# Optimization experiments

Measured on AMD Instinct MI355X. Metric: run time of the kernel, lower is better.

The kernel has to match this reference:

```python
import jax, jax.numpy as jnp
import numpy as np

N = 100_000      # nodes
E = 1_600_000    # directed edges (before self-loops)
F_IN = 128       # input node features
H = 4            # attention heads
C = 64           # hidden channels (concat=False -> heads averaged)
NEG_SLOPE = 0.2
BN_EPS = 1e-5


def setup_inputs() -> dict:
    key = jax.random.key(0)
    ks = jax.random.split(key, 16)
    s = 0.05
    return {
        "x": jax.random.normal(ks[0], (N, F_IN), dtype=jnp.float32),
        "edge_index": jax.random.randint(ks[1], (2, E), 0, N, dtype=jnp.int64),
        # GAT layer params: layer 0 has F_IN inputs, layers 1..2 have C inputs
        "W0": jax.random.normal(ks[2], (F_IN, H * C), dtype=jnp.float32) * s,
        "Wl": jax.random.normal(ks[3], (2, C, H * C), dtype=jnp.float32) * s,
        "att_src": jax.random.normal(ks[4], (3, H, C), dtype=jnp.float32) * s,
        "att_dst": jax.random.normal(ks[5], (3, H, C), dtype=jnp.float32) * s,
        "conv_bias": jnp.zeros((3, C), dtype=jnp.float32),
        # BatchNorm1d (inference: running stats)
        "bn_gamma": jnp.ones((3, C), dtype=jnp.float32),
        "bn_beta": jnp.zeros((3, C), dtype=jnp.float32),
        "bn_mean": jax.random.normal(ks[6], (3, C), dtype=jnp.float32) * 0.1,
        "bn_var": jax.random.uniform(ks[7], (3, C), dtype=jnp.float32, minval=0.5, maxval=1.5),
        # MLP head
        "lin1_w": jax.random.normal(ks[8], (C, C // 2), dtype=jnp.float32) * s,
        "lin1_b": jnp.zeros((C // 2,), dtype=jnp.float32),
        "lin2_w": jax.random.normal(ks[9], (C // 2, 1), dtype=jnp.float32) * s,
        "lin2_b": jnp.zeros((1,), dtype=jnp.float32),
    }


def _gat_layer(x, src, dst, W, a_src, a_dst, bias):
    # x: [N, Fin] -> h: [N, H, C]
    h = (x @ W).reshape(-1, H, C)
    # per-node attention logits, gathered per edge: [Etot, H]
    e_src = jnp.einsum("nhc,hc->nh", h, a_src)
    e_dst = jnp.einsum("nhc,hc->nh", h, a_dst)
    e = jax.nn.leaky_relu(e_src[src] + e_dst[dst], NEG_SLOPE)
    # softmax over incoming edges of each target node (self-loops guarantee non-empty)
    e_max = jax.ops.segment_max(e, dst, num_segments=N)
    w = jnp.exp(e - e_max[dst])                              # [Etot, H]
    denom = jax.ops.segment_sum(w, dst, num_segments=N)      # [N, H]
    # weighted scatter-add of gathered source features
    msg = h[src] * w[:, :, None]                             # [Etot, H, C]
    out = jax.ops.segment_sum(msg, dst, num_segments=N)      # [N, H, C]
    out = out / denom[:, :, None]
    return out.mean(axis=1) + bias                           # concat=False -> head mean


def reference(x, edge_index, W0, Wl, att_src, att_dst, conv_bias,
              bn_gamma, bn_beta, bn_mean, bn_var,
              lin1_w, lin1_b, lin2_w, lin2_b):
    # add self-loops (PyG GATConv default)
    loop = jnp.arange(N, dtype=edge_index.dtype)
    src = jnp.concatenate([edge_index[0], loop])
    dst = jnp.concatenate([edge_index[1], loop])

    Ws = [W0, Wl[0], Wl[1]]
    for l in range(3):
        x = _gat_layer(x, src, dst, Ws[l], att_src[l], att_dst[l], conv_bias[l])
        x = (x - bn_mean[l]) * (bn_gamma[l] / jnp.sqrt(bn_var[l] + BN_EPS)) + bn_beta[l]
        x = jax.nn.relu(x)  # dropout is identity in inference

    x = jax.nn.relu(x @ lin1_w + lin1_b)
    x = x @ lin2_w + lin2_b
    return x.squeeze(-1)
```

## Files before the change

### kernel.cpp

```cpp
#include <hip/hip_runtime.h>
#include <hip/hip_bf16.h>
#include <cstdint>

#define N_NODES 100000
#define N_EDGES 1600000
#define N_TOT   1700000
#define HEADS   4
#define CH      64
#define HC      256
#define NEG     0.2f
#define BNEPS   1e-5f
#define NPART   8
#define PART_N  12500
#define CHUNK_E 16384

typedef __attribute__((ext_vector_type(8))) short short8;
typedef __attribute__((ext_vector_type(4))) float f32x4;

static __device__ __forceinline__ float lrelu(float x) {
    return x > 0.f ? x : NEG * x;
}
static __device__ __forceinline__ unsigned short f2bf(float f) {
    unsigned int u = __float_as_uint(f);
    unsigned int r = (u + 0x7fffu + ((u >> 16) & 1u)) >> 16;
    return (unsigned short)r;
}
static __device__ __forceinline__ float bflo(unsigned int v) { return __uint_as_float(v << 16); }
static __device__ __forceinline__ float bfhi(unsigned int v) { return __uint_as_float(v & 0xffff0000u); }

__global__ void detect_dtype(const int* ei32, int* flag) {
    int l = threadIdx.x;
    int v = ei32[2 * l + 1];
    unsigned long long b = __ballot(v == 0);
    if (l == 0) *flag = (__popcll(b) >= 48) ? 1 : 0;
}

static __device__ __forceinline__ int edge_at(const void* ei, int is64, long long pos) {
    if (is64) return (int)((const long long*)ei)[pos];
    return ((const int*)ei)[pos];
}

__global__ void convert_hist_k(const void* ei, const int* flag,
                               int* __restrict__ src32, int* __restrict__ dst32,
                               int* __restrict__ counts) {
    int e = blockIdx.x * 256 + threadIdx.x;
    if (e >= N_TOT) return;
    int is64 = *flag;
    int s, d;
    if (e < N_EDGES) { s = edge_at(ei, is64, e); d = edge_at(ei, is64, (long long)N_EDGES + e); }
    else { int v = e - N_EDGES; s = v; d = v; }
    src32[e] = s; dst32[e] = d;
    atomicAdd(&counts[d], 1);
}

__global__ void scan_block(const int* in, int* out, int* bsum) {
    __shared__ int sm[256];
    int t = threadIdx.x;
    int i = blockIdx.x * 256 + t;
    int v = (i < N_NODES) ? in[i] : 0;
    int acc = v;
    sm[t] = v; __syncthreads();
    for (int d = 1; d < 256; d <<= 1) {
        int add = (t >= d) ? sm[t - d] : 0;
        __syncthreads();
        acc += add; sm[t] = acc;
        __syncthreads();
    }
    if (i < N_NODES) out[i] = acc - v;
    if (t == 255) bsum[blockIdx.x] = acc;
}

__global__ void scan_bsum(int* bsum, int nb) {
    __shared__ int sm[512];
    int t = threadIdx.x;
    int v = (t < nb) ? bsum[t] : 0;
    int acc = v;
    sm[t] = v; __syncthreads();
    for (int d = 1; d < 512; d <<= 1) {
        int add = (t >= d) ? sm[t - d] : 0;
        __syncthreads();
        acc += add; sm[t] = acc;
        __syncthreads();
    }
    if (t < nb) bsum[t] = acc - v;
}

__global__ void scan_add(int* off, const int* bsum, int* fill) {
    int i = blockIdx.x * 256 + threadIdx.x;
    if (i < N_NODES) {
        int v = off[i] + bsum[blockIdx.x];
        off[i] = v; fill[i] = v;
    }
    if (i == 0) off[N_NODES] = N_TOT;
}

__global__ void scatter_part_k(const int* __restrict__ src32, const int* __restrict__ dst32,
                               int* __restrict__ fill, int* __restrict__ csr) {
    int part = blockIdx.x & (NPART - 1), chunk = blockIdx.x / NPART;
    int lo = part * PART_N, hi = lo + PART_N;
    int base = chunk * CHUNK_E;
    int end = min(base + CHUNK_E, N_TOT);
    for (int i = base + threadIdx.x; i < end; i += 256) {
        int d = dst32[i];
        if (d >= lo && d < hi) {
            int s = src32[i];
            int pos = atomicAdd(&fill[d], 1);
            csr[pos] = s;
        }
    }
}

template<int K>
__global__ __launch_bounds__(256) void gemm_mfma_k(const float* __restrict__ A,
                                                   const float* __restrict__ Wf,
                                                   const float* __restrict__ as,
                                                   const float* __restrict__ ad,
                                                   unsigned short* __restrict__ hb,
                                                   float* __restrict__ es,
                                                   float* __restrict__ ed) {
    __shared__ unsigned short Bs[256 * K];
    __shared__ unsigned short As[64 * K];
    int t = threadIdx.x;
    int bm = blockIdx.x * 64;

    for (int idx4 = t; idx4 < K * 64; idx4 += 256) {
        int k = idx4 >> 6;
        int c = (idx4 & 63) * 4;
        float4 wv = *(const float4*)(Wf + (size_t)k * HC + c);
        Bs[((c + 0) * K + k) ^ ((((c + 0) & 7)) << 3)] = f2bf(wv.x);
        Bs[((c + 1) * K + k) ^ ((((c + 1) & 7)) << 3)] = f2bf(wv.y);
        Bs[((c + 2) * K + k) ^ ((((c + 2) & 7)) << 3)] = f2bf(wv.z);
        Bs[((c + 3) * K + k) ^ ((((c + 3) & 7)) << 3)] = f2bf(wv.w);
    }
    {
        int row = t >> 2, seg = t & 3;
        int grow = bm + row;
        const float* Ar = A + (size_t)grow * K + seg * (K / 4);
        #pragma unroll
        for (int f = 0; f < K / 16; ++f) {
            float4 v = make_float4(0.f, 0.f, 0.f, 0.f);
            if (grow < N_NODES) v = *(const float4*)(Ar + f * 4);
            ushort4 b;
            b.x = f2bf(v.x); b.y = f2bf(v.y); b.z = f2bf(v.z); b.w = f2bf(v.w);
            int idx = (row * K + seg * (K / 4) + f * 4) ^ ((row & 7) << 3);
            *(ushort4*)(&As[idx]) = b;
        }
    }
    __syncthreads();

    int w = t >> 6, lane = t & 63;
    int c16 = lane & 15, kg = lane >> 4;
    int swz = (c16 & 7) << 3;
    f32x4 acc[4][4];
    #pragma unroll
    for (int i = 0; i < 4; ++i)
        #pragma unroll
        for (int j = 0; j < 4; ++j) acc[i][j] = (f32x4)(0.f);

    #pragma unroll
    for (int kc = 0; kc < K / 32; ++kc) {
        int ko = kc * 32 + kg * 8;
        short8 af[4], bf[4];
        #pragma unroll
        for (int rs = 0; rs < 4; ++rs)
            af[rs] = *(const short8*)(&As[((16 * rs + c16) * K + ko) ^ swz]);
        #pragma unroll
        for (int ct = 0; ct < 4; ++ct) {
            int col = w * 64 + ct * 16 + c16;
            bf[ct] = *(const short8*)(&Bs[(col * K + ko) ^ swz]);
        }
        #pragma unroll
        for (int rs = 0; rs < 4; ++rs)
            #pragma unroll
            for (int ct = 0; ct < 4; ++ct)
                acc[rs][ct] = __builtin_amdgcn_mfma_f32_16x16x32_bf16(af[rs], bf[ct], acc[rs][ct], 0, 0, 0);
    }

    float asv[4], adv[4];
    #pragma unroll
    for (int ct = 0; ct < 4; ++ct) {
        asv[ct] = as[w * 64 + ct * 16 + c16];
        adv[ct] = ad[w * 64 + ct * 16 + c16];
    }
    #pragma unroll
    for (int rs = 0; rs < 4; ++rs) {
        float esr[4], edr[4];
        #pragma unroll
        for (int reg = 0; reg < 4; ++reg) {
            float s = 0.f, d = 0.f;
            #pragma unroll
            for (int ct = 0; ct < 4; ++ct) {
                s += acc[rs][ct][reg] * asv[ct];
                d += acc[rs][ct][reg] * adv[ct];
            }
            #pragma unroll
            for (int sh = 1; sh < 16; sh <<= 1) {
                s += __shfl_xor(s, sh);
                d += __shfl_xor(d, sh);
            }
            esr[reg] = s; edr[reg] = d;
        }
        int r0 = bm + rs * 16 + kg * 4;
        if (c16 == 0) {
            #pragma unroll
            for (int reg = 0; reg < 4; ++reg) {
                if (r0 + reg < N_NODES) {
                    es[(size_t)(r0 + reg) * 4 + w] = esr[reg];
                    ed[(size_t)(r0 + reg) * 4 + w] = edr[reg];
                }
            }
        }
        #pragma unroll
        for (int ct = 0; ct < 4; ++ct)
            #pragma unroll
            for (int reg = 0; reg < 4; ++reg) {
                int grow = r0 + reg;
                if (grow < N_NODES)
                    hb[(size_t)grow * HC + w * 64 + ct * 16 + c16] = f2bf(acc[rs][ct][reg]);
            }
    }
}

__global__ __launch_bounds__(256) void aggregate_k(const unsigned short* __restrict__ h,
                                                   const float* __restrict__ es,
                                                   const float* __restrict__ ed,
                                                   const int* __restrict__ off,
                                                   const int* __restrict__ csr,
                                                   const float* __restrict__ bias,
                                                   const float* __restrict__ g,
                                                   const float* __restrict__ bb,
                                                   const float* __restrict__ mu,
                                                   const float* __restrict__ var,
                                                   float* __restrict__ xout) {
    __shared__ float wbuf[4][64][4];
    __shared__ int   sbuf[4][64];
    int wv = threadIdx.x >> 6;
    int lane = threadIdx.x & 63;
    int wid = blockIdx.x * 4 + wv;
    if (wid >= N_NODES) return;

    int s0 = off[wid], s1 = off[wid + 1];
    float4 edv = *(const float4*)(ed + (size_t)wid * 4);

    int half = lane >> 5;
    int sub  = lane & 31;
    int head = sub >> 3;
    float ds0 = 0.f, ds1 = 0.f, ds2 = 0.f, ds3 = 0.f;
    float a0 = 0.f, a1 = 0.f, a2 = 0.f, a3 = 0.f, a4 = 0.f, a5 = 0.f, a6 = 0.f, a7 = 0.f;
    const unsigned short* hsub = h + sub * 8;

    for (int base = s0; base < s1; base += 64) {
        int e = base + lane;
        float w0 = 0.f, w1 = 0.f, w2 = 0.f, w3 = 0.f;
        int s = 0;
        if (e < s1) {
            s = csr[e];
            float4 ev = *(const float4*)(es + (size_t)s * 4);
            w0 = __expf(fminf(lrelu(ev.x + edv.x), 80.f));
            w1 = __expf(fminf(lrelu(ev.y + edv.y), 80.f));
            w2 = __expf(fminf(lrelu(ev.z + edv.z), 80.f));
            w3 = __expf(fminf(lrelu(ev.w + edv.w), 80.f));
        }
        ds0 += w0; ds1 += w1; ds2 += w2; ds3 += w3;
        *(float4*)(&wbuf[wv][lane][0]) = make_float4(w0, w1, w2, w3);
        sbuf[wv][lane] = s;
        asm volatile("" ::: "memory");

        int cnt = min(64, s1 - base);
        int jj = half;
        int scur = (jj < cnt) ? sbuf[wv][jj] : sbuf[wv][0];
        float wcur = (jj < cnt) ? wbuf[wv][jj][head] : 0.f;
        uint4 hv = *(const uint4*)(hsub + (size_t)scur * HC);
        for (int j = 0; j < cnt; j += 2) {
            int jn = j + 2 + half;
            int snx = (jn < cnt) ? sbuf[wv][jn] : sbuf[wv][0];
            float wnx = (jn < cnt) ? wbuf[wv][jn][head] : 0.f;
            uint4 hn = *(const uint4*)(hsub + (size_t)snx * HC);
            a0 = fmaf(wcur, bflo(hv.x), a0); a1 = fmaf(wcur, bfhi(hv.x), a1);
            a2 = fmaf(wcur, bflo(hv.y), a2); a3 = fmaf(wcur, bfhi(hv.y), a3);
            a4 = fmaf(wcur, bflo(hv.z), a4); a5 = fmaf(wcur, bfhi(hv.z), a5);
            a6 = fmaf(wcur, bflo(hv.w), a6); a7 = fmaf(wcur, bfhi(hv.w), a7);
            hv = hn; wcur = wnx;
        }
        asm volatile("" ::: "memory");
    }

    a0 += __shfl_xor(a0, 32); a1 += __shfl_xor(a1, 32);
    a2 += __shfl_xor(a2, 32); a3 += __shfl_xor(a3, 32);
    a4 += __shfl_xor(a4, 32); a5 += __shfl_xor(a5, 32);
    a6 += __shfl_xor(a6, 32); a7 += __shfl_xor(a7, 32);

    #pragma unroll
    for (int d = 1; d < 64; d <<= 1) {
        ds0 += __shfl_xor(ds0, d); ds1 += __shfl_xor(ds1, d);
        ds2 += __shfl_xor(ds2, d); ds3 += __shfl_xor(ds3, d);
    }
    float den = head == 0 ? ds0 : head == 1 ? ds1 : head == 2 ? ds2 : ds3;
    float inv = 1.f / den;
    a0 *= inv; a1 *= inv; a2 *= inv; a3 *= inv;
    a4 *= inv; a5 *= inv; a6 *= inv; a7 *= inv;

    a0 += __shfl_xor(a0, 8);  a1 += __shfl_xor(a1, 8);
    a2 += __shfl_xor(a2, 8);  a3 += __shfl_xor(a3, 8);
    a4 += __shfl_xor(a4, 8);  a5 += __shfl_xor(a5, 8);
    a6 += __shfl_xor(a6, 8);  a7 += __shfl_xor(a7, 8);
    a0 += __shfl_xor(a0, 16); a1 += __shfl_xor(a1, 16);
    a2 += __shfl_xor(a2, 16); a3 += __shfl_xor(a3, 16);
    a4 += __shfl_xor(a4, 16); a5 += __shfl_xor(a5, 16);
    a6 += __shfl_xor(a6, 16); a7 += __shfl_xor(a7, 16);

    if (lane < 8) {
        int c = lane * 8;
        float av[8] = {a0, a1, a2, a3, a4, a5, a6, a7};
        float4 bi0 = *(const float4*)(bias + c), bi1 = *(const float4*)(bias + c + 4);
        float4 gv0 = *(const float4*)(g + c),    gv1 = *(const float4*)(g + c + 4);
        float4 bv0 = *(const float4*)(bb + c),   bv1 = *(const float4*)(bb + c + 4);
        float4 mv0 = *(const float4*)(mu + c),   mv1 = *(const float4*)(mu + c + 4);
        float4 vv0 = *(const float4*)(var + c),  vv1 = *(const float4*)(var + c + 4);
        float bia[8] = {bi0.x, bi0.y, bi0.z, bi0.w, bi1.x, bi1.y, bi1.z, bi1.w};
        float gg[8]  = {gv0.x, gv0.y, gv0.z, gv0.w, gv1.x, gv1.y, gv1.z, gv1.w};
        float be[8]  = {bv0.x, bv0.y, bv0.z, bv0.w, bv1.x, bv1.y, bv1.z, bv1.w};
        float mm[8]  = {mv0.x, mv0.y, mv0.z, mv0.w, mv1.x, mv1.y, mv1.z, mv1.w};
        float vv[8]  = {vv0.x, vv0.y, vv0.z, vv0.w, vv1.x, vv1.y, vv1.z, vv1.w};
        float o[8];
        #pragma unroll
        for (int k = 0; k < 8; ++k) {
            float t0 = (av[k] * 0.25f + bia[k] - mm[k]) * (gg[k] * rsqrtf(vv[k] + BNEPS)) + be[k];
            o[k] = fmaxf(t0, 0.f);
        }
        *(float4*)(xout + (size_t)wid * CH + c)     = make_float4(o[0], o[1], o[2], o[3]);
        *(float4*)(xout + (size_t)wid * CH + c + 4) = make_float4(o[4], o[5], o[6], o[7]);
    }
}

__global__ __launch_bounds__(256) void mlp_k(const float* __restrict__ x,
                                             const float* __restrict__ w1,
                                             const float* __restrict__ b1,
                                             const float* __restrict__ w2,
                                             const float* __restrict__ b2,
                                             float* __restrict__ out) {
    __shared__ float w1s[CH * 32];
    __shared__ float w2s[32];
    __shared__ float b1s[32];
    int t = threadIdx.x;
    for (int i = t; i < CH * 32; i += 256) w1s[i] = w1[i];
    if (t < 32) { w2s[t] = w2[t]; b1s[t] = b1[t]; }
    __syncthreads();
    int n = blockIdx.x * 256 + t;
    if (n >= N_NODES) return;
    float y[32];
    #pragma unroll
    for (int j = 0; j < 32; ++j) y[j] = b1s[j];
    const float* xr = x + (size_t)n * CH;
    for (int c4 = 0; c4 < 16; ++c4) {
        float4 xv = *(const float4*)(xr + c4 * 4);
        const float* wr = &w1s[c4 * 4 * 32];
        #pragma unroll
        for (int j = 0; j < 32; ++j)
            y[j] += xv.x * wr[j] + xv.y * wr[32 + j] + xv.z * wr[64 + j] + xv.w * wr[96 + j];
    }
    float o = b2[0];
    #pragma unroll
    for (int j = 0; j < 32; ++j) o += fmaxf(y[j], 0.f) * w2s[j];
    out[n] = o;
}

extern "C" void kernel_launch(void* const* d_in, const int* in_sizes, int n_in,
                              void* d_out, int out_size, void* d_ws, size_t ws_size,
                              hipStream_t stream) {
    const float* x0    = (const float*)d_in[0];
    const void*  ei    = d_in[1];
    const float* W0    = (const float*)d_in[2];
    const float* Wl    = (const float*)d_in[3];
    const float* asrc  = (const float*)d_in[4];
    const float* adst  = (const float*)d_in[5];
    const float* cbias = (const float*)d_in[6];
    const float* bng   = (const float*)d_in[7];
    const float* bnb   = (const float*)d_in[8];
    const float* bnm   = (const float*)d_in[9];
    const float* bnv   = (const float*)d_in[10];
    const float* l1w   = (const float*)d_in[11];
    const float* l1b   = (const float*)d_in[12];
    const float* l2w   = (const float*)d_in[13];
    const float* l2b   = (const float*)d_in[14];
    float* out = (float*)d_out;

    char* p = (char*)d_ws;
    auto alloc = [&](size_t bytes) { char* r = p; p += (bytes + 255) & ~(size_t)255; return r; };
    unsigned short* hb  = (unsigned short*)alloc((size_t)N_NODES * HC * 2);
    float* xA   = (float*)alloc((size_t)N_NODES * CH * 4);
    float* xB   = (float*)alloc((size_t)N_NODES * CH * 4);
    float* es   = (float*)alloc((size_t)N_NODES * 4 * 4);
    float* ed   = (float*)alloc((size_t)N_NODES * 4 * 4);
    int* counts = (int*)alloc((size_t)N_NODES * 4);
    int* off    = (int*)alloc((size_t)(N_NODES + 1) * 4);
    int* fill   = (int*)alloc((size_t)N_NODES * 4);
    int* bsum   = (int*)alloc(512 * 4);
    int* flag   = (int*)alloc(256);
    int* src32  = (int*)alloc((size_t)N_TOT * 4);
    int* dst32  = (int*)alloc((size_t)N_TOT * 4);
    int* csr    = (int*)alloc((size_t)N_TOT * 4);

    int nbScan = (N_NODES + 255) / 256;
    int nchunk = (N_TOT + CHUNK_E - 1) / CHUNK_E;
    hipMemsetAsync(counts, 0, (size_t)N_NODES * 4, stream);
    detect_dtype<<<1, 64, 0, stream>>>((const int*)ei, flag);
    convert_hist_k<<<(N_TOT + 255) / 256, 256, 0, stream>>>(ei, flag, src32, dst32, counts);
    scan_block<<<nbScan, 256, 0, stream>>>(counts, off, bsum);
    scan_bsum<<<1, 512, 0, stream>>>(bsum, nbScan);
    scan_add<<<nbScan, 256, 0, stream>>>(off, bsum, fill);
    scatter_part_k<<<nchunk * NPART, 256, 0, stream>>>(src32, dst32, fill, csr);

    const float* xin = x0;
    const float* W = W0;
    float* xbufs[2] = {xA, xB};
    int ngemm = (N_NODES + 63) / 64;
    for (int l = 0; l < 3; ++l) {
        if (l == 0)
            gemm_mfma_k<128><<<ngemm, 256, 0, stream>>>(xin, W, asrc + l * HC, adst + l * HC, hb, es, ed);
        else
            gemm_mfma_k<64><<<ngemm, 256, 0, stream>>>(xin, W, asrc + l * HC, adst + l * HC, hb, es, ed);
        float* xo = xbufs[l & 1];
        aggregate_k<<<(N_NODES + 3) / 4, 256, 0, stream>>>(hb, es, ed, off, csr,
            cbias + l * CH, bng + l * CH, bnb + l * CH, bnm + l * CH, bnv + l * CH, xo);
        xin = xo;
        W = Wl + (size_t)l * CH * HC;
    }
    mlp_k<<<(N_NODES + 255) / 256, 256, 0, stream>>>(xin, l1w, l1b, l2w, l2b, out);
}
```

Baseline: 747.4 us.

## Persistent GEMM with bf16 intermediate activations, coalesced h stores, fused dtype detect

Makes the GEMM kernel persistent (grid-stride over row tiles) so the bf16 weight tile in shared memory is converted once per block instead of once per tile. The h output is staged through shared memory so it can be written with 16-byte stores, where each lane previously wrote one 2-byte value. Aggregation for layers 0 and 1 now writes bf16 activations that the next GEMM reads directly, halving that traffic and removing the float-to-bf16 conversion. The separate dtype-detect kernel is folded into the edge conversion kernel, dropping one launch. The cost is extra barriers per tile and bf16 rounding of intermediate activations.

```diff
diff --git a/kernel.cpp b/kernel.cpp
--- a/kernel.cpp
+++ b/kernel.cpp
@@ -28,27 +28,26 @@
 static __device__ __forceinline__ float bflo(unsigned int v) { return __uint_as_float(v << 16); }
 static __device__ __forceinline__ float bfhi(unsigned int v) { return __uint_as_float(v & 0xffff0000u); }
 
-__global__ void detect_dtype(const int* ei32, int* flag) {
-    int l = threadIdx.x;
-    int v = ei32[2 * l + 1];
-    unsigned long long b = __ballot(v == 0);
-    if (l == 0) *flag = (__popcll(b) >= 48) ? 1 : 0;
-}
-
-static __device__ __forceinline__ int edge_at(const void* ei, int is64, long long pos) {
-    if (is64) return (int)((const long long*)ei)[pos];
-    return ((const int*)ei)[pos];
-}
-
-__global__ void convert_hist_k(const void* ei, const int* flag,
+__global__ void convert_hist_k(const void* ei,
                                int* __restrict__ src32, int* __restrict__ dst32,
                                int* __restrict__ counts) {
+    const int* e32 = (const int*)ei;
+    int l = threadIdx.x & 63;
+    unsigned long long b = __ballot(e32[2 * l + 1] == 0);
+    int is64 = (__popcll(b) >= 48) ? 1 : 0;
+
     int e = blockIdx.x * 256 + threadIdx.x;
     if (e >= N_TOT) return;
-    int is64 = *flag;
     int s, d;
-    if (e < N_EDGES) { s = edge_at(ei, is64, e); d = edge_at(ei, is64, (long long)N_EDGES + e); }
-    else { int v = e - N_EDGES; s = v; d = v; }
+    if (e < N_EDGES) {
+        if (is64) {
+            s = (int)((const long long*)ei)[e];
+            d = (int)((const long long*)ei)[(long long)N_EDGES + e];
+        } else {
+            s = ((const int*)ei)[e];
+            d = ((const int*)ei)[N_EDGES + e];
+        }
+    } else { int v = e - N_EDGES; s = v; d = v; }
     src32[e] = s; dst32[e] = d;
     atomicAdd(&counts[d], 1);
 }
@@ -110,117 +109,143 @@
     }
 }
 
-template<int K>
-__global__ __launch_bounds__(256) void gemm_mfma_k(const float* __restrict__ A,
+template<int K, bool ABF16>
+__global__ __launch_bounds__(256) void gemm_mfma_k(const void* __restrict__ Ain,
                                                    const float* __restrict__ Wf,
                                                    const float* __restrict__ as,
                                                    const float* __restrict__ ad,
                                                    unsigned short* __restrict__ hb,
                                                    float* __restrict__ es,
-                                                   float* __restrict__ ed) {
-    __shared__ unsigned short Bs[256 * K];
-    __shared__ unsigned short As[64 * K];
+                                                   float* __restrict__ ed, int ntiles) {
+    __shared__ __align__(16) unsigned short Bs[256 * K];
+    __shared__ __align__(16) unsigned short As[64 * K];
     int t = threadIdx.x;
-    int bm = blockIdx.x * 64;
 
     for (int idx4 = t; idx4 < K * 64; idx4 += 256) {
         int k = idx4 >> 6;
         int c = (idx4 & 63) * 4;
         float4 wv = *(const float4*)(Wf + (size_t)k * HC + c);
-        Bs[((c + 0) * K + k) ^ ((((c + 0) & 7)) << 3)] = f2bf(wv.x);
-        Bs[((c + 1) * K + k) ^ ((((c + 1) & 7)) << 3)] = f2bf(wv.y);
-        Bs[((c + 2) * K + k) ^ ((((c + 2) & 7)) << 3)] = f2bf(wv.z);
-        Bs[((c + 3) * K + k) ^ ((((c + 3) & 7)) << 3)] = f2bf(wv.w);
-    }
-    {
-        int row = t >> 2, seg = t & 3;
-        int grow = bm + row;
-        const float* Ar = A + (size_t)grow * K + seg * (K / 4);
-        #pragma unroll
-        for (int f = 0; f < K / 16; ++f) {
-            float4 v = make_float4(0.f, 0.f, 0.f, 0.f);
-            if (grow < N_NODES) v = *(const float4*)(Ar + f * 4);
-            ushort4 b;
-            b.x = f2bf(v.x); b.y = f2bf(v.y); b.z = f2bf(v.z); b.w = f2bf(v.w);
-            int idx = (row * K + seg * (K / 4) + f * 4) ^ ((row & 7) << 3);
-            *(ushort4*)(&As[idx]) = b;
-        }
-    }
-    __syncthreads();
+        Bs[((c + 0) * K + k) ^ (((c + 0) & 7) << 3)] = f2bf(wv.x);
+        Bs[((c + 1) * K + k) ^ (((c + 1) & 7) << 3)] = f2bf(wv.y);
+        Bs[((c + 2) * K + k) ^ (((c + 2) & 7) << 3)] = f2bf(wv.z);
+        Bs[((c + 3) * K + k) ^ (((c + 3) & 7) << 3)] = f2bf(wv.w);
+    }
 
     int w = t >> 6, lane = t & 63;
     int c16 = lane & 15, kg = lane >> 4;
     int swz = (c16 & 7) << 3;
-    f32x4 acc[4][4];
-    #pragma unroll
-    for (int i = 0; i < 4; ++i)
-        #pragma unroll
-        for (int j = 0; j < 4; ++j) acc[i][j] = (f32x4)(0.f);
-
-    #pragma unroll
-    for (int kc = 0; kc < K / 32; ++kc) {
-        int ko = kc * 32 + kg * 8;
-        short8 af[4], bf[4];
-        #pragma unroll
-        for (int rs = 0; rs < 4; ++rs)
-            af[rs] = *(const short8*)(&As[((16 * rs + c16) * K + ko) ^ swz]);
-        #pragma unroll
-        for (int ct = 0; ct < 4; ++ct) {
-            int col = w * 64 + ct * 16 + c16;
-            bf[ct] = *(const short8*)(&Bs[(col * K + ko) ^ swz]);
-        }
-        #pragma unroll
-        for (int rs = 0; rs < 4; ++rs)
-            #pragma unroll
-            for (int ct = 0; ct < 4; ++ct)
-                acc[rs][ct] = __builtin_amdgcn_mfma_f32_16x16x32_bf16(af[rs], bf[ct], acc[rs][ct], 0, 0, 0);
-    }
-
     float asv[4], adv[4];
     #pragma unroll
     for (int ct = 0; ct < 4; ++ct) {
         asv[ct] = as[w * 64 + ct * 16 + c16];
         adv[ct] = ad[w * 64 + ct * 16 + c16];
     }
-    #pragma unroll
-    for (int rs = 0; rs < 4; ++rs) {
-        float esr[4], edr[4];
-        #pragma unroll
-        for (int reg = 0; reg < 4; ++reg) {
-            float s = 0.f, d = 0.f;
-            #pragma unroll
-            for (int ct = 0; ct < 4; ++ct) {
-                s += acc[rs][ct][reg] * asv[ct];
-                d += acc[rs][ct][reg] * adv[ct];
-            }
-            #pragma unroll
-            for (int sh = 1; sh < 16; sh <<= 1) {
-                s += __shfl_xor(s, sh);
-                d += __shfl_xor(d, sh);
-            }
-            esr[reg] = s; edr[reg] = d;
-        }
-        int r0 = bm + rs * 16 + kg * 4;
-        if (c16 == 0) {
-            #pragma unroll
-            for (int reg = 0; reg < 4; ++reg) {
-                if (r0 + reg < N_NODES) {
-                    es[(size_t)(r0 + reg) * 4 + w] = esr[reg];
-                    ed[(size_t)(r0 + reg) * 4 + w] = edr[reg];
+    __syncthreads();
+
+    for (int tile = blockIdx.x; tile < ntiles; tile += gridDim.x) {
+        int bm = tile * 64;
+        #pragma unroll
+        for (int i = 0; i < (64 * K / 8) / 256; ++i) {
+            int cidx = i * 256 + t;
+            int row = cidx / (K / 8);
+            int ks = (cidx % (K / 8)) * 8;
+            int grow = bm + row;
+            uint4 pk = make_uint4(0, 0, 0, 0);
+            if (grow < N_NODES) {
+                if (ABF16) {
+                    pk = *(const uint4*)((const unsigned short*)Ain + (size_t)grow * K + ks);
+                } else {
+                    const float* Af = (const float*)Ain + (size_t)grow * K + ks;
+                    float4 v0 = *(const float4*)Af;
+                    float4 v1 = *(const float4*)(Af + 4);
+                    pk.x = (unsigned)f2bf(v0.x) | ((unsigned)f2bf(v0.y) << 16);
+                    pk.y = (unsigned)f2bf(v0.z) | ((unsigned)f2bf(v0.w) << 16);
+                    pk.z = (unsigned)f2bf(v1.x) | ((unsigned)f2bf(v1.y) << 16);
+                    pk.w = (unsigned)f2bf(v1.z) | ((unsigned)f2bf(v1.w) << 16);
                 }
             }
-        }
-        #pragma unroll
-        for (int ct = 0; ct < 4; ++ct)
+            *(uint4*)(&As[(row * K + ks) ^ ((row & 7) << 3)]) = pk;
+        }
+        __syncthreads();
+
+        f32x4 acc[4][4];
+        #pragma unroll
+        for (int i = 0; i < 4; ++i)
+            #pragma unroll
+            for (int j = 0; j < 4; ++j) acc[i][j] = (f32x4)(0.f);
+
+        #pragma unroll
+        for (int kc = 0; kc < K / 32; ++kc) {
+            int ko = kc * 32 + kg * 8;
+            short8 af[4], bf[4];
+            #pragma unroll
+            for (int rs = 0; rs < 4; ++rs)
+                af[rs] = *(const short8*)(&As[((16 * rs + c16) * K + ko) ^ swz]);
+            #pragma unroll
+            for (int ct = 0; ct < 4; ++ct) {
+                int col = w * 64 + ct * 16 + c16;
+                bf[ct] = *(const short8*)(&Bs[(col * K + ko) ^ swz]);
+            }
+            #pragma unroll
+            for (int rs = 0; rs < 4; ++rs)
+                #pragma unroll
+                for (int ct = 0; ct < 4; ++ct)
+                    acc[rs][ct] = __builtin_amdgcn_mfma_f32_16x16x32_bf16(af[rs], bf[ct], acc[rs][ct], 0, 0, 0);
+        }
+
+        #pragma unroll
+        for (int rs = 0; rs < 4; ++rs) {
+            float esr[4], edr[4];
             #pragma unroll
             for (int reg = 0; reg < 4; ++reg) {
-                int grow = r0 + reg;
-                if (grow < N_NODES)
-                    hb[(size_t)grow * HC + w * 64 + ct * 16 + c16] = f2bf(acc[rs][ct][reg]);
+                float s = 0.f, d = 0.f;
+                #pragma unroll
+                for (int ct = 0; ct < 4; ++ct) {
+                    s += acc[rs][ct][reg] * asv[ct];
+                    d += acc[rs][ct][reg] * adv[ct];
+                }
+                #pragma unroll
+                for (int sh = 1; sh < 16; sh <<= 1) {
+                    s += __shfl_xor(s, sh);
+                    d += __shfl_xor(d, sh);
+                }
+                esr[reg] = s; edr[reg] = d;
             }
-    }
-}
-
+            if (c16 == 0) {
+                int r0 = bm + rs * 16 + kg * 4;
+                #pragma unroll
+                for (int reg = 0; reg < 4; ++reg) {
+                    if (r0 + reg < N_NODES) {
+                        es[(size_t)(r0 + reg) * 4 + w] = esr[reg];
+                        ed[(size_t)(r0 + reg) * 4 + w] = edr[reg];
+                    }
+                }
+            }
+        }
+        __syncthreads();
+
+        #pragma unroll
+        for (int rs = 0; rs < 4; ++rs) {
+            #pragma unroll
+            for (int ct = 0; ct < 4; ++ct)
+                #pragma unroll
+                for (int reg = 0; reg < 4; ++reg)
+                    As[(kg * 4 + reg) * 256 + w * 64 + ct * 16 + c16] = f2bf(acc[rs][ct][reg]);
+            __syncthreads();
+            int row16 = t >> 4, cseg = (t & 15) * 16;
+            int grow = bm + rs * 16 + row16;
+            if (grow < N_NODES) {
+                uint4 v0 = *(const uint4*)(&As[row16 * 256 + cseg]);
+                uint4 v1 = *(const uint4*)(&As[row16 * 256 + cseg + 8]);
+                *(uint4*)(hb + (size_t)grow * HC + cseg) = v0;
+                *(uint4*)(hb + (size_t)grow * HC + cseg + 8) = v1;
+            }
+            __syncthreads();
+        }
+    }
+}
+
+template<bool OUTBF16>
 __global__ __launch_bounds__(256) void aggregate_k(const unsigned short* __restrict__ h,
                                                    const float* __restrict__ es,
                                                    const float* __restrict__ ed,
@@ -231,7 +256,7 @@
                                                    const float* __restrict__ bb,
                                                    const float* __restrict__ mu,
                                                    const float* __restrict__ var,
-                                                   float* __restrict__ xout) {
+                                                   void* __restrict__ xout) {
     __shared__ float wbuf[4][64][4];
     __shared__ int   sbuf[4][64];
     int wv = threadIdx.x >> 6;
@@ -328,8 +353,17 @@
             float t0 = (av[k] * 0.25f + bia[k] - mm[k]) * (gg[k] * rsqrtf(vv[k] + BNEPS)) + be[k];
             o[k] = fmaxf(t0, 0.f);
         }
-        *(float4*)(xout + (size_t)wid * CH + c)     = make_float4(o[0], o[1], o[2], o[3]);
-        *(float4*)(xout + (size_t)wid * CH + c + 4) = make_float4(o[4], o[5], o[6], o[7]);
+        if (OUTBF16) {
+            uint4 pk;
+            pk.x = (unsigned)f2bf(o[0]) | ((unsigned)f2bf(o[1]) << 16);
+            pk.y = (unsigned)f2bf(o[2]) | ((unsigned)f2bf(o[3]) << 16);
+            pk.z = (unsigned)f2bf(o[4]) | ((unsigned)f2bf(o[5]) << 16);
+            pk.w = (unsigned)f2bf(o[6]) | ((unsigned)f2bf(o[7]) << 16);
+            *(uint4*)((unsigned short*)xout + (size_t)wid * CH + c) = pk;
+        } else {
+            *(float4*)((float*)xout + (size_t)wid * CH + c)     = make_float4(o[0], o[1], o[2], o[3]);
+            *(float4*)((float*)xout + (size_t)wid * CH + c + 4) = make_float4(o[4], o[5], o[6], o[7]);
+        }
     }
 }
 
@@ -387,44 +421,40 @@
 
     char* p = (char*)d_ws;
     auto alloc = [&](size_t bytes) { char* r = p; p += (bytes + 255) & ~(size_t)255; return r; };
-    unsigned short* hb  = (unsigned short*)alloc((size_t)N_NODES * HC * 2);
-    float* xA   = (float*)alloc((size_t)N_NODES * CH * 4);
-    float* xB   = (float*)alloc((size_t)N_NODES * CH * 4);
+    unsigned short* hb   = (unsigned short*)alloc((size_t)N_NODES * HC * 2);
+    unsigned short* xb0  = (unsigned short*)alloc((size_t)N_NODES * CH * 2);
+    unsigned short* xb1  = (unsigned short*)alloc((size_t)N_NODES * CH * 2);
+    float* xf32 = (float*)alloc((size_t)N_NODES * CH * 4);
     float* es   = (float*)alloc((size_t)N_NODES * 4 * 4);
     float* ed   = (float*)alloc((size_t)N_NODES * 4 * 4);
     int* counts = (int*)alloc((size_t)N_NODES * 4);
     int* off    = (int*)alloc((size_t)(N_NODES + 1) * 4);
     int* fill   = (int*)alloc((size_t)N_NODES * 4);
     int* bsum   = (int*)alloc(512 * 4);
-    int* flag   = (int*)alloc(256);
     int* src32  = (int*)alloc((size_t)N_TOT * 4);
     int* dst32  = (int*)alloc((size_t)N_TOT * 4);
     int* csr    = (int*)alloc((size_t)N_TOT * 4);
 
     int nbScan = (N_NODES + 255) / 256;
     int nchunk = (N_TOT + CHUNK_E - 1) / CHUNK_E;
+    int ntiles = (N_NODES + 63) / 64;
     hipMemsetAsync(counts, 0, (size_t)N_NODES * 4, stream);
-    detect_dtype<<<1, 64, 0, stream>>>((const int*)ei, flag);
-    convert_hist_k<<<(N_TOT + 255) / 256, 256, 0, stream>>>(ei, flag, src32, dst32, counts);
+    convert_hist_k<<<(N_TOT + 255) / 256, 256, 0, stream>>>(ei, src32, dst32, counts);
     scan_block<<<nbScan, 256, 0, stream>>>(counts, off, bsum);
     scan_bsum<<<1, 512, 0, stream>>>(bsum, nbScan);
     scan_add<<<nbScan, 256, 0, stream>>>(off, bsum, fill);
     scatter_part_k<<<nchunk * NPART, 256, 0, stream>>>(src32, dst32, fill, csr);
 
-    const float* xin = x0;
-    const float* W = W0;
-    float* xbufs[2] = {xA, xB};
-    int ngemm = (N_NODES + 63) / 64;
-    for (int l = 0; l < 3; ++l) {
-        if (l == 0)
-            gemm_mfma_k<128><<<ngemm, 256, 0, stream>>>(xin, W, asrc + l * HC, adst + l * HC, hb, es, ed);
-        else
-            gemm_mfma_k<64><<<ngemm, 256, 0, stream>>>(xin, W, asrc + l * HC, adst + l * HC, hb, es, ed);
-        float* xo = xbufs[l & 1];
-        aggregate_k<<<(N_NODES + 3) / 4, 256, 0, stream>>>(hb, es, ed, off, csr,
-            cbias + l * CH, bng + l * CH, bnb + l * CH, bnm + l * CH, bnv + l * CH, xo);
-        xin = xo;
-        W = Wl + (size_t)l * CH * HC;
-    }
-    mlp_k<<<(N_NODES + 255) / 256, 256, 0, stream>>>(xin, l1w, l1b, l2w, l2b, out);
-}
+    int nagg = (N_NODES + 3) / 4;
+    gemm_mfma_k<128, false><<<512, 256, 0, stream>>>(x0, W0, asrc, adst, hb, es, ed, ntiles);
+    aggregate_k<true><<<nagg, 256, 0, stream>>>(hb, es, ed, off, csr,
+        cbias, bng, bnb, bnm, bnv, xb0);
+    gemm_mfma_k<64, true><<<1024, 256, 0, stream>>>(xb0, Wl, asrc + HC, adst + HC, hb, es, ed, ntiles);
+    aggregate_k<true><<<nagg, 256, 0, stream>>>(hb, es, ed, off, csr,
+        cbias + CH, bng + CH, bnb + CH, bnm + CH, bnv + CH, xb1);
+    gemm_mfma_k<64, true><<<1024, 256, 0, stream>>>(xb1, Wl + (size_t)CH * HC, asrc + 2 * HC, adst + 2 * HC, hb, es, ed, ntiles);
+    aggregate_k<false><<<nagg, 256, 0, stream>>>(hb, es, ed, off, csr,
+        cbias + 2 * CH, bng + 2 * CH, bnb + 2 * CH, bnm + 2 * CH, bnv + 2 * CH, xf32);
+
+    mlp_k<<<(N_NODES + 255) / 256, 256, 0, stream>>>(xf32, l1w, l1b, l2w, l2b, out);
+}
```

New measurement: 698.5 us. 1.07x faster.
